# Kernel tuning notes

Hardware: AMD Instinct MI355X
Metric: run time of the kernel (lower is better)

## Reference

```python
import jax, jax.numpy as jnp
import numpy as np

B, T, D, H = 8, 2048, 512, 2048
EPS = 1e-5


def setup_inputs() -> dict:
    key = jax.random.key(0)
    ks = jax.random.split(key, 12)
    s_d = 1.0 / np.sqrt(D)
    s_h = 1.0 / np.sqrt(H)
    s_w = np.sqrt(6.0 / (T + T))  # xavier_uniform scale for w [T,T]
    return {
        "x": jax.random.normal(ks[0], (B, T, D), jnp.float32),
        "ln1_g": jnp.ones((D,), jnp.float32),
        "ln1_b": jnp.zeros((D,), jnp.float32),
        "Wk": jax.random.normal(ks[1], (D, D), jnp.float32) * s_d,
        "bk": jnp.zeros((D,), jnp.float32),
        "Wv": jax.random.normal(ks[2], (D, D), jnp.float32) * s_d,
        "bv": jnp.zeros((D,), jnp.float32),
        "Wq": jax.random.normal(ks[3], (D, D), jnp.float32) * s_d,
        "bq": jnp.zeros((D,), jnp.float32),
        "w": jax.random.uniform(ks[4], (T, T), jnp.float32, -s_w, s_w),
        "Wo": jax.random.normal(ks[5], (D, D), jnp.float32) * s_d,
        "bo": jnp.zeros((D,), jnp.float32),
        "ln2_g": jnp.ones((D,), jnp.float32),
        "ln2_b": jnp.zeros((D,), jnp.float32),
        "W1": jax.random.normal(ks[6], (D, H), jnp.float32) * s_d,
        "b1": jnp.zeros((H,), jnp.float32),
        "W2": jax.random.normal(ks[7], (H, D), jnp.float32) * s_h,
        "b2": jnp.zeros((D,), jnp.float32),
    }


def _ln(x, g, b):
    mu = jnp.mean(x, axis=-1, keepdims=True)
    var = jnp.mean(jnp.square(x - mu), axis=-1, keepdims=True)
    return (x - mu) * jax.lax.rsqrt(var + EPS) * g + b


def _aft_full(h, Wk, bk, Wv, bv, Wq, bq, w, Wo, bo):
    # h: [B,T,D]
    K = h @ Wk + bk
    V = h @ Wv + bv
    # row-max stabilized position bias [T,T]
    exp_w = jnp.exp(w - jnp.max(w, axis=-1, keepdims=True))
    # NOTE: original stabilizes K with max over dim=0 (the BATCH dim) -- faithful
    exp_K = jnp.exp(K - jnp.max(K, axis=0, keepdims=True))  # [B,T,D]
    num = jnp.einsum("ts,bsd->btd", exp_w, exp_K * V)
    den = jnp.einsum("ts,bsd->btd", exp_w, exp_K)
    Yt = num / den
    Q = h @ Wq + bq
    Yt = jax.nn.sigmoid(Q) * Yt
    return Yt @ Wo + bo


def reference(x, ln1_g, ln1_b, Wk, bk, Wv, bv, Wq, bq, w, Wo, bo,
              ln2_g, ln2_b, W1, b1, W2, b2):
    attn = _aft_full(_ln(x, ln1_g, ln1_b), Wk, bk, Wv, bv, Wq, bq, w, Wo, bo)
    out = attn + x
    h = _ln(out, ln2_g, ln2_b)
    h = jax.nn.gelu(h @ W1 + b1, approximate=False)
    h = jax.nn.gelu(h @ W2 + b2, approximate=False)  # GELU after 2nd linear too (faithful)
    return h + out
```

## Files before the change

kernel.cpp:

```cpp
#include <hip/hip_runtime.h>
#include <hip/hip_bf16.h>
#include <math.h>

typedef __hip_bfloat16 bf16;
typedef __bf16 bf16x8 __attribute__((ext_vector_type(8)));
typedef float f32x4 __attribute__((ext_vector_type(4)));

#define B_ 8
#define T_ 2048
#define D_ 512
#define H_ 2048

__device__ __forceinline__ float b2f(unsigned short u) {
    return __uint_as_float((unsigned)u << 16);
}
__device__ __forceinline__ float ldf(const float* p, long i) { return p[i]; }
__device__ __forceinline__ float ldf(const bf16* p, long i) {
    return b2f(((const unsigned short*)p)[i]);
}
__device__ __forceinline__ float gelu_f(float v) {
    float a = 1.5957691216057308f * (v + 0.044715f * v * v * v);
    return v / (1.0f + __expf(-a));
}

__device__ __forceinline__ long poff(int row, int col, int K) {
    return ((long)(row >> 4) * (K >> 5) + (col >> 5)) * 512 + (row & 15) * 32 + (col & 31);
}

#define GLD16(g, l)                                                          \
    __builtin_amdgcn_global_load_lds(                                        \
        (const __attribute__((address_space(1))) void*)(g),                  \
        (__attribute__((address_space(3))) void*)(l), 16, 0, 0)

template <typename Tin, bool PACKO>
__global__ __launch_bounds__(256) void ln_kernel(const Tin* __restrict__ x,
                                                 const float* __restrict__ g,
                                                 const float* __restrict__ bb,
                                                 bf16* __restrict__ y) {
    int row = blockIdx.x;
    long base = (long)row * D_;
    int tid = threadIdx.x;
    float v0 = ldf(x, base + tid);
    float v1 = ldf(x, base + tid + 256);
    float s = v0 + v1;
#pragma unroll
    for (int off = 32; off > 0; off >>= 1) s += __shfl_down(s, off);
    __shared__ float red[4];
    int lane = tid & 63, wid = tid >> 6;
    if (lane == 0) red[wid] = s;
    __syncthreads();
    float mean = (red[0] + red[1] + red[2] + red[3]) * (1.0f / 512.0f);
    __syncthreads();
    float d0 = v0 - mean, d1 = v1 - mean;
    float vs = d0 * d0 + d1 * d1;
#pragma unroll
    for (int off = 32; off > 0; off >>= 1) vs += __shfl_down(vs, off);
    if (lane == 0) red[wid] = vs;
    __syncthreads();
    float var = (red[0] + red[1] + red[2] + red[3]) * (1.0f / 512.0f);
    float rstd = rsqrtf(var + 1e-5f);
    float o0 = d0 * rstd * g[tid] + bb[tid];
    float o1 = d1 * rstd * g[tid + 256] + bb[tid + 256];
    if (PACKO) {
        y[poff(row, tid, D_)]       = __float2bfloat16(o0);
        y[poff(row, tid + 256, D_)] = __float2bfloat16(o1);
    } else {
        y[base + tid]       = __float2bfloat16(o0);
        y[base + tid + 256] = __float2bfloat16(o1);
    }
}

__global__ __launch_bounds__(256) void expw_kernel(const float* __restrict__ w,
                                                   bf16* __restrict__ ew) {
    int row = blockIdx.x;
    long base = (long)row * T_;
    int tid = threadIdx.x;
    float v[8];
    float mx = -3.4e38f;
#pragma unroll
    for (int i = 0; i < 8; ++i) {
        v[i] = w[base + tid + i * 256];
        mx = fmaxf(mx, v[i]);
    }
#pragma unroll
    for (int off = 32; off > 0; off >>= 1) mx = fmaxf(mx, __shfl_down(mx, off));
    __shared__ float red[4];
    if ((tid & 63) == 0) red[tid >> 6] = mx;
    __syncthreads();
    float rmax = fmaxf(fmaxf(red[0], red[1]), fmaxf(red[2], red[3]));
#pragma unroll
    for (int i = 0; i < 8; ++i)
        ew[poff(row, tid + i * 256, T_)] = __float2bfloat16(expf(v[i] - rmax));
}

__global__ __launch_bounds__(256) void maxk_kernel(const bf16* __restrict__ K,
                                                   bf16* __restrict__ mk) {
    long i = (long)blockIdx.x * 256 + threadIdx.x;
    float m = ldf(K, i);
#pragma unroll
    for (int b = 1; b < B_; ++b) m = fmaxf(m, ldf(K, (long)b * (T_ * D_) + i));
    mk[i] = __float2bfloat16(m);
}

__global__ __launch_bounds__(256) void kv2t_kernel(const bf16* __restrict__ K_,
                                                   const bf16* __restrict__ V_,
                                                   const bf16* __restrict__ mk,
                                                   bf16* __restrict__ kv2t) {
    __shared__ float sev[64][65];
    __shared__ float se[64][65];
    int tx = threadIdx.x & 63, ty = threadIdx.x >> 6;
    int t0 = blockIdx.x * 64, d0 = blockIdx.y * 64, b = blockIdx.z;
    long ibase = (long)b << 20;
#pragma unroll
    for (int r = 0; r < 16; ++r) {
        int tl = r * 4 + ty;
        long mi = (long)(t0 + tl) * D_ + d0 + tx;
        float e = expf(ldf(K_, ibase + mi) - ldf(mk, mi));
        sev[tl][tx] = e * ldf(V_, ibase + mi);
        se[tl][tx] = e;
    }
    __syncthreads();
    long obase = (long)b << 21;
#pragma unroll
    for (int r = 0; r < 16; ++r) {
        int dl = r * 4 + ty;
        int nrow = 2 * (d0 + dl);
        kv2t[obase + poff(nrow,     t0 + tx, T_)] = __float2bfloat16(sev[tx][dl]);
        kv2t[obase + poff(nrow + 1, t0 + tx, T_)] = __float2bfloat16(se[tx][dl]);
    }
}

struct WT6 {
    const float* src[6];
    bf16* dst[6];
    int K[6], N[6];
};
__global__ __launch_bounds__(256) void wtrans6_kernel(WT6 p) {
    int z = blockIdx.z;
    int K = p.K[z], N = p.N[z];
    int n0 = blockIdx.x * 64, k0 = blockIdx.y * 64;
    if (n0 >= N || k0 >= K) return;
    const float* W = p.src[z];
    bf16* WT = p.dst[z];
    __shared__ float s[64][65];
    int tx = threadIdx.x & 63, ty = threadIdx.x >> 6;
#pragma unroll
    for (int r = 0; r < 16; ++r) {
        int kl = r * 4 + ty;
        s[kl][tx] = W[(long)(k0 + kl) * N + n0 + tx];
    }
    __syncthreads();
#pragma unroll
    for (int r = 0; r < 16; ++r) {
        int nl = r * 4 + ty;
        WT[poff(n0 + nl, k0 + tx, K)] = __float2bfloat16(s[tx][nl]);
    }
}

template <int BM, int PK>
__global__ __launch_bounds__(256, 4) void mfma_gemm(
    const bf16* __restrict__ A, const bf16* __restrict__ Bt,
    const float* __restrict__ b0, const float* __restrict__ b1,
    const float* __restrict__ b2,
    bf16* __restrict__ Cb, float* __restrict__ Cf,
    const bf16* __restrict__ resb, const float* __restrict__ resf,
    bf16* __restrict__ yq,
    int M, int N, int K, int modes, long bsB, long bsC, long planeStride) {
    constexpr int MI = BM / 32;
    constexpr int NA = BM / 64;
    constexpr int PL = (BM + 128) * 32;
    constexpr bool PA = PK & 1, PB = PK & 2, PCK = PK & 4;
    constexpr long astep = PA ? 512 : 32;
    constexpr long bstep = PB ? 512 : 32;
    __shared__ short Sh[2 * PL];
    int tid = threadIdx.x;
    int lane = tid & 63, wave = tid >> 6;
    int wm = wave & 1, wn = wave >> 1;

    int gx = gridDim.x, gy = gridDim.y;
    long nwg = (long)gx * gy * gridDim.z;
    long o = blockIdx.x + (long)gx * (blockIdx.y + (long)gy * blockIdx.z);
    long wk = (o & 7) * (nwg >> 3) + (o >> 3);
    int bx = (int)(wk % gx);
    long rq = wk / gx;
    int by = (int)(rq % gy);
    int bz = (int)(rq / gy);
    int m0 = by * BM, n0 = bx * 128;

    const short* Ag = (const short*)A;
    const short* Bg = (const short*)Bt + (long)bz * bsB;

    int lr = lane >> 2;
    int le = (lane & 3) * 8;
    const short* ga[NA];
    short* la[NA];
#pragma unroll
    for (int i = 0; i < NA; ++i) {
        int arow = m0 + wave * (BM / 4) + i * 16;
        ga[i] = PA ? Ag + (long)(arow >> 4) * ((long)K << 4) + lane * 8
                   : Ag + (long)(arow + lr) * K + le;
        la[i] = Sh + (wave * (BM / 4) + i * 16) * 32;
    }
    int brow = n0 + wave * 32;
    const short* gb0 = PB ? Bg + (long)(brow >> 4) * ((long)K << 4) + lane * 8
                          : Bg + (long)(brow + lr) * K + le;
    const short* gb1 = PB ? gb0 + ((long)K << 4) : gb0 + 16L * K;
    short* lb0 = Sh + BM * 32 + (wave * 32) * 32;
    short* lb1 = lb0 + 16 * 32;

    f32x4 acc[MI][4];
    f32x4 zz = {0.f, 0.f, 0.f, 0.f};
#pragma unroll
    for (int i = 0; i < MI; ++i)
#pragma unroll
        for (int j = 0; j < 4; ++j) acc[i][j] = zz;

    int fr = lane & 15;
    int fk = (lane >> 4) * 8;
    int rm = wm * (BM / 2);

    auto stage = [&](int kt, int ofs) {
#pragma unroll
        for (int i = 0; i < NA; ++i) GLD16(ga[i] + kt * astep, la[i] + ofs);
        GLD16(gb0 + kt * bstep, lb0 + ofs);
        GLD16(gb1 + kt * bstep, lb1 + ofs);
    };
    auto compute = [&](int ofs) {
        const short* Asb = Sh + ofs;
        const short* Bsb = Sh + ofs + BM * 32;
        bf16x8 af[MI], bv[4];
#pragma unroll
        for (int mi = 0; mi < MI; ++mi)
            af[mi] = *(const bf16x8*)(Asb + (rm + mi * 16 + fr) * 32 + fk);
#pragma unroll
        for (int ni = 0; ni < 4; ++ni)
            bv[ni] = *(const bf16x8*)(Bsb + (wn * 64 + ni * 16 + fr) * 32 + fk);
#pragma unroll
        for (int mi = 0; mi < MI; ++mi)
#pragma unroll
            for (int ni = 0; ni < 4; ++ni)
                acc[mi][ni] = __builtin_amdgcn_mfma_f32_16x16x32_bf16(
                    af[mi], bv[ni], acc[mi][ni], 0, 0, 0);
    };

    int nk = K >> 5;
    stage(0, 0);
    __syncthreads();
    for (int kt = 0; kt < nk; kt += 2) {
        if (kt + 1 < nk) stage(kt + 1, PL);
        compute(0);
        __syncthreads();
        if (kt + 2 < nk) stage(kt + 2, 0);
        compute(PL);
        __syncthreads();
    }

    int cc = lane & 15, cr = (lane >> 4) * 4;
    if (yq) {
        long qb = (long)bz * (long)(T_ * D_);
#pragma unroll
        for (int mi = 0; mi < MI; ++mi) {
#pragma unroll
            for (int ni = 0; ni < 4; ++ni) {
                int row0 = m0 + rm + mi * 16 + cr;
                int col = n0 + wn * 64 + ni * 16 + cc;
                int d = col >> 1;
#pragma unroll
                for (int r = 0; r < 4; ++r) {
                    float v = acc[mi][ni][r];
                    float other = __shfl_xor(v, 1);
                    if (!(lane & 1)) {
                        long qi = qb + (long)(row0 + r) * D_ + d;
                        float sq = ldf((const bf16*)yq, qi);
                        yq[qi] = __float2bfloat16(sq * v / other);
                    }
                }
            }
        }
        return;
    }
    long cbase = (long)bz * bsC;
#pragma unroll
    for (int mi = 0; mi < MI; ++mi) {
#pragma unroll
        for (int ni = 0; ni < 4; ++ni) {
            int row0 = m0 + rm + mi * 16 + cr;
            int col = n0 + wn * 64 + ni * 16 + cc;
            float bvl;
            long colterm;
            int md, rowstride;
            if (planeStride) {
                int plane = col >> 9;
                int c2 = col & 511;
                const float* bp = (plane == 0) ? b0 : ((plane == 1) ? b1 : b2);
                bvl = bp[c2];
                md = (modes >> (2 * plane)) & 3;
                colterm = (long)plane * planeStride + c2;
                rowstride = 512;
            } else {
                bvl = b0 ? b0[col] : 0.0f;
                md = modes & 3;
                colterm = col;
                rowstride = N;
            }
#pragma unroll
            for (int r = 0; r < 4; ++r) {
                float v = acc[mi][ni][r] + bvl;
                if (md == 1) v = 1.0f / (1.0f + __expf(-v));
                else if (md == 2) v = gelu_f(v);
                long idx;
                if (PCK) idx = cbase + poff(row0 + r, col, N);
                else     idx = cbase + (long)(row0 + r) * rowstride + colterm;
                if (resf) v += resf[idx];
                if (resb) v += ldf(resb, idx);
                if (Cf) Cf[idx] = v;
                else Cb[idx] = __float2bfloat16(v);
            }
        }
    }
}

extern "C" void kernel_launch(void* const* d_in, const int* in_sizes, int n_in,
                              void* d_out, int out_size, void* d_ws, size_t ws_size,
                              hipStream_t stream) {
    const float* x    = (const float*)d_in[0];
    const float* ln1g = (const float*)d_in[1];
    const float* ln1b = (const float*)d_in[2];
    const float* Wk   = (const float*)d_in[3];
    const float* bk   = (const float*)d_in[4];
    const float* Wv   = (const float*)d_in[5];
    const float* bv   = (const float*)d_in[6];
    const float* Wq   = (const float*)d_in[7];
    const float* bq   = (const float*)d_in[8];
    const float* w    = (const float*)d_in[9];
    const float* Wo   = (const float*)d_in[10];
    const float* bo   = (const float*)d_in[11];
    const float* ln2g = (const float*)d_in[12];
    const float* ln2b = (const float*)d_in[13];
    const float* W1   = (const float*)d_in[14];
    const float* b1   = (const float*)d_in[15];
    const float* W2   = (const float*)d_in[16];
    const float* b2   = (const float*)d_in[17];
    float* out = (float*)d_out;

    const long S_BTD = (long)B_ * T_ * D_;
    const long S_TD  = (long)T_ * D_;
    const long S_TT  = (long)T_ * T_;
    const long S_B2D = (long)B_ * T_ * 2 * D_;
    const long S_DD  = (long)D_ * D_;

    bf16* h1     = (bf16*)d_ws;
    bf16* outres = h1 + S_BTD;
    bf16* ew     = outres + S_BTD;
    bf16* KVQ    = ew + S_TT;
    bf16* kv2t   = KVQ + 3 * S_BTD;
    bf16* mk     = kv2t + S_B2D;
    bf16* WkT    = mk + 2 * S_TD;
    bf16* WvT    = WkT + S_DD;
    bf16* WqT    = WvT + S_DD;
    bf16* WoT    = WqT + S_DD;
    bf16* W1T    = WoT + S_DD;
    bf16* W2T    = W1T + (long)D_ * H_;
    bf16* Kb  = KVQ;
    bf16* Vb  = KVQ + S_BTD;
    bf16* Qb  = KVQ + 2 * S_BTD;
    bf16* hH  = KVQ;
    bf16* h2  = h1;

    const int M = B_ * T_;

    WT6 p;
    p.src[0] = Wk; p.src[1] = Wv; p.src[2] = Wq; p.src[3] = Wo; p.src[4] = W1; p.src[5] = W2;
    p.dst[0] = WkT; p.dst[1] = WvT; p.dst[2] = WqT; p.dst[3] = WoT; p.dst[4] = W1T; p.dst[5] = W2T;
    p.K[0] = p.K[1] = p.K[2] = p.K[3] = 512; p.K[4] = 512; p.K[5] = 2048;
    p.N[0] = p.N[1] = p.N[2] = p.N[3] = 512; p.N[4] = 2048; p.N[5] = 512;
    wtrans6_kernel<<<dim3(32, 32, 6), 256, 0, stream>>>(p);
    ln_kernel<float, true><<<M, 256, 0, stream>>>(x, ln1g, ln1b, h1);
    mfma_gemm<128, 3><<<dim3(1536 / 128, M / 128, 1), 256, 0, stream>>>(
        h1, WkT, bk, bv, bq, Kb, nullptr, nullptr, nullptr, nullptr,
        M, 1536, D_, (1 << 4), 0, 0, S_BTD);
    maxk_kernel<<<S_TD / 256, 256, 0, stream>>>(Kb, mk);
    kv2t_kernel<<<dim3(T_ / 64, D_ / 64, B_), 256, 0, stream>>>(Kb, Vb, mk, kv2t);
    expw_kernel<<<T_, 256, 0, stream>>>(w, ew);
    mfma_gemm<128, 3><<<dim3(1024 / 128, T_ / 128, B_), 256, 0, stream>>>(
        ew, kv2t, nullptr, nullptr, nullptr, nullptr, nullptr, nullptr, nullptr, Qb,
        T_, 1024, T_, 0, (long)1024 * T_, 0, 0);
    mfma_gemm<128, 2><<<dim3(D_ / 128, M / 128, 1), 256, 0, stream>>>(
        Qb, WoT, bo, nullptr, nullptr, outres, nullptr, nullptr, x, nullptr,
        M, D_, D_, 0, 0, 0, 0);
    ln_kernel<bf16, true><<<M, 256, 0, stream>>>(outres, ln2g, ln2b, h2);
    mfma_gemm<128, 7><<<dim3(H_ / 128, M / 128, 1), 256, 0, stream>>>(
        h2, W1T, b1, nullptr, nullptr, hH, nullptr, nullptr, nullptr, nullptr,
        M, H_, D_, 2, 0, 0, 0);
    mfma_gemm<128, 3><<<dim3(D_ / 128, M / 128, 1), 256, 0, stream>>>(
        hH, W2T, b2, nullptr, nullptr, nullptr, out, outres, nullptr, nullptr,
        M, D_, H_, 2, 0, 0, 0);
}
```

Baseline: 486.4 us.

## Fuse prep kernels and merge batch-max with KV packing, simplify AFT epilogue

Merges weight transpose, first layernorm and exp(w) into a single prep launch, and folds the batch-dim max of K into the KV exp/transpose kernel, which now loops over all batches itself. This removes the mk intermediate buffer and several launches. The kv2t row interleaving changes from pairwise (num, den) to 16-row blocks, so the num/den epilogue can divide accumulators held in the same lane instead of using a lane shuffle. The risk is that mkv now runs only 256 blocks and reads K twice, which lowers parallelism for that stage.

```diff
diff --git a/kernel.cpp b/kernel.cpp
--- a/kernel.cpp
+++ b/kernel.cpp
@@ -33,19 +33,17 @@
         (__attribute__((address_space(3))) void*)(l), 16, 0, 0)
 
 template <typename Tin, bool PACKO>
-__global__ __launch_bounds__(256) void ln_kernel(const Tin* __restrict__ x,
-                                                 const float* __restrict__ g,
-                                                 const float* __restrict__ bb,
-                                                 bf16* __restrict__ y) {
-    int row = blockIdx.x;
+__device__ __forceinline__ void ln_body(const Tin* __restrict__ x,
+                                        const float* __restrict__ g,
+                                        const float* __restrict__ bb,
+                                        bf16* __restrict__ y, int row, int tid,
+                                        float* red) {
     long base = (long)row * D_;
-    int tid = threadIdx.x;
     float v0 = ldf(x, base + tid);
     float v1 = ldf(x, base + tid + 256);
     float s = v0 + v1;
 #pragma unroll
     for (int off = 32; off > 0; off >>= 1) s += __shfl_down(s, off);
-    __shared__ float red[4];
     int lane = tid & 63, wid = tid >> 6;
     if (lane == 0) red[wid] = s;
     __syncthreads();
@@ -70,64 +68,13 @@
     }
 }
 
-__global__ __launch_bounds__(256) void expw_kernel(const float* __restrict__ w,
-                                                   bf16* __restrict__ ew) {
-    int row = blockIdx.x;
-    long base = (long)row * T_;
-    int tid = threadIdx.x;
-    float v[8];
-    float mx = -3.4e38f;
-#pragma unroll
-    for (int i = 0; i < 8; ++i) {
-        v[i] = w[base + tid + i * 256];
-        mx = fmaxf(mx, v[i]);
-    }
-#pragma unroll
-    for (int off = 32; off > 0; off >>= 1) mx = fmaxf(mx, __shfl_down(mx, off));
+template <typename Tin, bool PACKO>
+__global__ __launch_bounds__(256) void ln_kernel(const Tin* __restrict__ x,
+                                                 const float* __restrict__ g,
+                                                 const float* __restrict__ bb,
+                                                 bf16* __restrict__ y) {
     __shared__ float red[4];
-    if ((tid & 63) == 0) red[tid >> 6] = mx;
-    __syncthreads();
-    float rmax = fmaxf(fmaxf(red[0], red[1]), fmaxf(red[2], red[3]));
-#pragma unroll
-    for (int i = 0; i < 8; ++i)
-        ew[poff(row, tid + i * 256, T_)] = __float2bfloat16(expf(v[i] - rmax));
-}
-
-__global__ __launch_bounds__(256) void maxk_kernel(const bf16* __restrict__ K,
-                                                   bf16* __restrict__ mk) {
-    long i = (long)blockIdx.x * 256 + threadIdx.x;
-    float m = ldf(K, i);
-#pragma unroll
-    for (int b = 1; b < B_; ++b) m = fmaxf(m, ldf(K, (long)b * (T_ * D_) + i));
-    mk[i] = __float2bfloat16(m);
-}
-
-__global__ __launch_bounds__(256) void kv2t_kernel(const bf16* __restrict__ K_,
-                                                   const bf16* __restrict__ V_,
-                                                   const bf16* __restrict__ mk,
-                                                   bf16* __restrict__ kv2t) {
-    __shared__ float sev[64][65];
-    __shared__ float se[64][65];
-    int tx = threadIdx.x & 63, ty = threadIdx.x >> 6;
-    int t0 = blockIdx.x * 64, d0 = blockIdx.y * 64, b = blockIdx.z;
-    long ibase = (long)b << 20;
-#pragma unroll
-    for (int r = 0; r < 16; ++r) {
-        int tl = r * 4 + ty;
-        long mi = (long)(t0 + tl) * D_ + d0 + tx;
-        float e = expf(ldf(K_, ibase + mi) - ldf(mk, mi));
-        sev[tl][tx] = e * ldf(V_, ibase + mi);
-        se[tl][tx] = e;
-    }
-    __syncthreads();
-    long obase = (long)b << 21;
-#pragma unroll
-    for (int r = 0; r < 16; ++r) {
-        int dl = r * 4 + ty;
-        int nrow = 2 * (d0 + dl);
-        kv2t[obase + poff(nrow,     t0 + tx, T_)] = __float2bfloat16(sev[tx][dl]);
-        kv2t[obase + poff(nrow + 1, t0 + tx, T_)] = __float2bfloat16(se[tx][dl]);
-    }
+    ln_body<Tin, PACKO>(x, g, bb, y, blockIdx.x, threadIdx.x, red);
 }
 
 struct WT6 {
@@ -135,25 +82,99 @@
     bf16* dst[6];
     int K[6], N[6];
 };
-__global__ __launch_bounds__(256) void wtrans6_kernel(WT6 p) {
-    int z = blockIdx.z;
-    int K = p.K[z], N = p.N[z];
-    int n0 = blockIdx.x * 64, k0 = blockIdx.y * 64;
-    if (n0 >= N || k0 >= K) return;
-    const float* W = p.src[z];
-    bf16* WT = p.dst[z];
-    __shared__ float s[64][65];
+
+__global__ __launch_bounds__(256) void prep_kernel(WT6 p,
+                                                   const float* __restrict__ x,
+                                                   const float* __restrict__ ln1g,
+                                                   const float* __restrict__ ln1b,
+                                                   bf16* __restrict__ h1,
+                                                   const float* __restrict__ w,
+                                                   bf16* __restrict__ ew) {
+    __shared__ float sbuf[64][65];
+    int bid = blockIdx.x;
+    int tid = threadIdx.x;
+    if (bid < 6144) {
+        int z = bid >> 10;
+        int rem = bid & 1023;
+        int n0 = (rem & 31) * 64, k0 = (rem >> 5) * 64;
+        int K = p.K[z], N = p.N[z];
+        if (n0 >= N || k0 >= K) return;
+        const float* W = p.src[z];
+        bf16* WT = p.dst[z];
+        int tx = tid & 63, ty = tid >> 6;
+#pragma unroll
+        for (int r = 0; r < 16; ++r) {
+            int kl = r * 4 + ty;
+            sbuf[kl][tx] = W[(long)(k0 + kl) * N + n0 + tx];
+        }
+        __syncthreads();
+#pragma unroll
+        for (int r = 0; r < 16; ++r) {
+            int nl = r * 4 + ty;
+            WT[poff(n0 + nl, k0 + tx, K)] = __float2bfloat16(sbuf[tx][nl]);
+        }
+    } else if (bid < 6144 + 16384) {
+        ln_body<float, true>(x, ln1g, ln1b, h1, bid - 6144, tid, &sbuf[0][0]);
+    } else {
+        int row = bid - (6144 + 16384);
+        long base = (long)row * T_;
+        float v[8];
+        float mx = -3.4e38f;
+#pragma unroll
+        for (int i = 0; i < 8; ++i) {
+            v[i] = w[base + tid + i * 256];
+            mx = fmaxf(mx, v[i]);
+        }
+#pragma unroll
+        for (int off = 32; off > 0; off >>= 1) mx = fmaxf(mx, __shfl_down(mx, off));
+        float* red = &sbuf[0][0];
+        if ((tid & 63) == 0) red[tid >> 6] = mx;
+        __syncthreads();
+        float rmax = fmaxf(fmaxf(red[0], red[1]), fmaxf(red[2], red[3]));
+#pragma unroll
+        for (int i = 0; i < 8; ++i)
+            ew[poff(row, tid + i * 256, T_)] = __float2bfloat16(expf(v[i] - rmax));
+    }
+}
+
+__global__ __launch_bounds__(256) void mkv_kernel(const bf16* __restrict__ K_,
+                                                  const bf16* __restrict__ V_,
+                                                  bf16* __restrict__ kv2t) {
+    __shared__ float sev[64][65];
+    __shared__ float se[64][65];
     int tx = threadIdx.x & 63, ty = threadIdx.x >> 6;
-#pragma unroll
-    for (int r = 0; r < 16; ++r) {
-        int kl = r * 4 + ty;
-        s[kl][tx] = W[(long)(k0 + kl) * N + n0 + tx];
-    }
-    __syncthreads();
-#pragma unroll
-    for (int r = 0; r < 16; ++r) {
-        int nl = r * 4 + ty;
-        WT[poff(n0 + nl, k0 + tx, K)] = __float2bfloat16(s[tx][nl]);
+    int t0 = blockIdx.x * 64, d0 = blockIdx.y * 64;
+    float mx[16];
+#pragma unroll
+    for (int r = 0; r < 16; ++r) mx[r] = -3.4e38f;
+    for (int b = 0; b < B_; ++b) {
+        long ibase = (long)b << 20;
+#pragma unroll
+        for (int r = 0; r < 16; ++r) {
+            long mi = (long)(t0 + r * 4 + ty) * D_ + d0 + tx;
+            mx[r] = fmaxf(mx[r], ldf(K_, ibase + mi));
+        }
+    }
+    for (int b = 0; b < B_; ++b) {
+        long ibase = (long)b << 20;
+#pragma unroll
+        for (int r = 0; r < 16; ++r) {
+            int tl = r * 4 + ty;
+            long mi = (long)(t0 + tl) * D_ + d0 + tx;
+            float e = expf(ldf(K_, ibase + mi) - mx[r]);
+            sev[tl][tx] = e * ldf(V_, ibase + mi);
+            se[tl][tx] = e;
+        }
+        __syncthreads();
+        long obase = (long)b << 21;
+#pragma unroll
+        for (int r = 0; r < 16; ++r) {
+            int d = d0 + r * 4 + ty;
+            int nrow = ((d >> 4) << 5) + (d & 15);
+            kv2t[obase + poff(nrow,      t0 + tx, T_)] = __float2bfloat16(sev[tx][r * 4 + ty]);
+            kv2t[obase + poff(nrow + 16, t0 + tx, T_)] = __float2bfloat16(se[tx][r * 4 + ty]);
+        }
+        __syncthreads();
     }
 }
 
@@ -258,22 +279,19 @@
     int cc = lane & 15, cr = (lane >> 4) * 4;
     if (yq) {
         long qb = (long)bz * (long)(T_ * D_);
+        int dbase = (n0 + wn * 64) >> 1;
 #pragma unroll
         for (int mi = 0; mi < MI; ++mi) {
-#pragma unroll
-            for (int ni = 0; ni < 4; ++ni) {
-                int row0 = m0 + rm + mi * 16 + cr;
-                int col = n0 + wn * 64 + ni * 16 + cc;
-                int d = col >> 1;
+            int row0 = m0 + rm + mi * 16 + cr;
+#pragma unroll
+            for (int pp = 0; pp < 2; ++pp) {
+                int d = dbase + pp * 16 + cc;
 #pragma unroll
                 for (int r = 0; r < 4; ++r) {
-                    float v = acc[mi][ni][r];
-                    float other = __shfl_xor(v, 1);
-                    if (!(lane & 1)) {
-                        long qi = qb + (long)(row0 + r) * D_ + d;
-                        float sq = ldf((const bf16*)yq, qi);
-                        yq[qi] = __float2bfloat16(sq * v / other);
-                    }
+                    long qi = qb + (long)(row0 + r) * D_ + d;
+                    float sq = ldf((const bf16*)yq, qi);
+                    yq[qi] = __float2bfloat16(sq * acc[mi][2 * pp][r] /
+                                              acc[mi][2 * pp + 1][r]);
                 }
             }
         }
@@ -374,14 +392,12 @@
     p.dst[0] = WkT; p.dst[1] = WvT; p.dst[2] = WqT; p.dst[3] = WoT; p.dst[4] = W1T; p.dst[5] = W2T;
     p.K[0] = p.K[1] = p.K[2] = p.K[3] = 512; p.K[4] = 512; p.K[5] = 2048;
     p.N[0] = p.N[1] = p.N[2] = p.N[3] = 512; p.N[4] = 2048; p.N[5] = 512;
-    wtrans6_kernel<<<dim3(32, 32, 6), 256, 0, stream>>>(p);
-    ln_kernel<float, true><<<M, 256, 0, stream>>>(x, ln1g, ln1b, h1);
+
+    prep_kernel<<<6144 + 16384 + 2048, 256, 0, stream>>>(p, x, ln1g, ln1b, h1, w, ew);
     mfma_gemm<128, 3><<<dim3(1536 / 128, M / 128, 1), 256, 0, stream>>>(
         h1, WkT, bk, bv, bq, Kb, nullptr, nullptr, nullptr, nullptr,
         M, 1536, D_, (1 << 4), 0, 0, S_BTD);
-    maxk_kernel<<<S_TD / 256, 256, 0, stream>>>(Kb, mk);
-    kv2t_kernel<<<dim3(T_ / 64, D_ / 64, B_), 256, 0, stream>>>(Kb, Vb, mk, kv2t);
-    expw_kernel<<<T_, 256, 0, stream>>>(w, ew);
+    mkv_kernel<<<dim3(T_ / 64, D_ / 64), 256, 0, stream>>>(Kb, Vb, kv2t);
     mfma_gemm<128, 3><<<dim3(1024 / 128, T_ / 128, B_), 256, 0, stream>>>(
         ew, kv2t, nullptr, nullptr, nullptr, nullptr, nullptr, nullptr, nullptr, Qb,
         T_, 1024, T_, 0, (long)1024 * T_, 0, 0);
```

After: 522.4 us. 1.07x slower.
